# Kernel tuning notes

Measured on AMD Instinct MI355X. Metric: run time of the kernel, lower is better.

## Reference

```python
import jax, jax.numpy as jnp
import numpy as np

N = 200000      # nodes (Elliptic-like AML graph)
E = 400000      # edges
F_IN = 165      # num_features
H = 512         # hidden_units
C = 2           # num_classes


def setup_inputs() -> dict:
    key = jax.random.key(0)
    ks = jax.random.split(key, 10)

    def glorot(k, shape):
        fan_in = shape[0]
        return (jax.random.normal(k, shape, jnp.float32) / np.float32(np.sqrt(fan_in)))

    return {
        "x": jax.random.normal(ks[0], (N, F_IN), jnp.float32),
        "edge_index": jax.random.randint(ks[1], (2, E), 0, N, dtype=jnp.int32),
        # ChebConv1: K=2 -> two weight mats + one bias
        "W1_0": glorot(ks[2], (F_IN, H)),
        "W1_1": glorot(ks[3], (F_IN, H)),
        "b1": jnp.zeros((H,), jnp.float32),
        # ChebConv2: K=2
        "W2_0": glorot(ks[4], (H, H)),
        "W2_1": glorot(ks[5], (H, H)),
        "b2": jnp.zeros((H,), jnp.float32),
        # final Linear
        "Wl": glorot(ks[6], (H, C)),
        "bl": jnp.zeros((C,), jnp.float32),
    }


def _edge_norm(src, dst, n, dtype):
    # Scaled Chebyshev Laplacian L_hat = 2L/lambda_max - I with sym norm and
    # lambda_max=2 (PyG defaults): diagonal is 0, off-diag = -D^{-1/2} A D^{-1/2}.
    ones = jnp.ones(src.shape[0], dtype)
    deg = jax.ops.segment_sum(ones, src, num_segments=n)
    dis = jnp.where(deg > 0, jax.lax.rsqrt(jnp.where(deg > 0, deg, 1.0)), 0.0)
    return -dis[src] * dis[dst]  # [E]


def _prop(h, src, dst, w, n):
    # One application of L_hat: gather -> weight -> scatter-add. [E, F] messages.
    return jax.ops.segment_sum(w[:, None] * h[src], dst, num_segments=n)


def reference(x, edge_index, W1_0, W1_1, b1, W2_0, W2_1, b2, Wl, bl):
    n = x.shape[0]
    src, dst = edge_index[0], edge_index[1]
    w = _edge_norm(src, dst, n, x.dtype)
    # ChebConv K=2: out = Tx0 @ W0 + Tx1 @ W1 + b, Tx1 = L_hat x
    h = jax.nn.relu(x @ W1_0 + _prop(x, src, dst, w, n) @ W1_1 + b1)
    h = jax.nn.relu(h @ W2_0 + _prop(h, src, dst, w, n) @ W2_1 + b2)
    return h @ Wl + bl  # [N, C] logits
```

## Files before the change

### kernel.cpp

```cpp
#include <hip/hip_runtime.h>

#define NNODES 200000
#define MPAD   200064
#define NEDGES 400000
#define FIN    165
#define K1P    192
#define HID    512
#define NB     ((NNODES + 255) / 256)

typedef __bf16 bf16_t;
typedef __bf16 bf16x8 __attribute__((ext_vector_type(8)));
typedef float  f32x4  __attribute__((ext_vector_type(4)));
typedef unsigned short su16x8 __attribute__((ext_vector_type(8)));
typedef float f32x4u __attribute__((ext_vector_type(4), aligned(4)));

static __device__ __forceinline__ float bf2f(unsigned short u) {
    unsigned int x = ((unsigned int)u) << 16;
    return __builtin_bit_cast(float, x);
}
static __device__ __forceinline__ unsigned short f2bf(float f) {
    bf16_t h = (bf16_t)f;
    return __builtin_bit_cast(unsigned short, h);
}
static __device__ __forceinline__ void gl_lds16(const void* g, void* l) {
    __builtin_amdgcn_global_load_lds(
        (const __attribute__((address_space(1))) unsigned int*)g,
        (__attribute__((address_space(3))) unsigned int*)l, 16, 0, 0);
}
static __device__ __forceinline__ int xcd_swz(int i, int nb) {
    int q = nb >> 3, r = nb & 7;
    int xcd = i & 7, seq = i >> 3;
    return (xcd < r ? xcd * (q + 1) : r * (q + 1) + (xcd - r) * q) + seq;
}

__global__ void k_deg(const int* __restrict__ src, const int* __restrict__ dst,
                      int* __restrict__ deg, int* __restrict__ cnt, int E) {
    int e = blockIdx.x * 256 + threadIdx.x;
    if (e < E) {
        atomicAdd(&deg[src[e]], 1);
        atomicAdd(&cnt[dst[e]], 1);
    }
}

__global__ void k_scan1(int* __restrict__ cnt, int* __restrict__ btot, int n) {
    __shared__ int s[256];
    int i = blockIdx.x * 256 + threadIdx.x;
    int v = (i < n) ? cnt[i] : 0;
    s[threadIdx.x] = v;
    __syncthreads();
    #pragma unroll
    for (int off = 1; off < 256; off <<= 1) {
        int t = (threadIdx.x >= off) ? s[threadIdx.x - off] : 0;
        __syncthreads();
        s[threadIdx.x] += t;
        __syncthreads();
    }
    if (i < n) cnt[i] = s[threadIdx.x] - v;
    if (threadIdx.x == 255) btot[blockIdx.x] = s[255];
}

__global__ void k_scan2(int* __restrict__ btot, int nb) {
    __shared__ int s[1024];
    int i = threadIdx.x;
    int v = (i < nb) ? btot[i] : 0;
    s[i] = v;
    __syncthreads();
    #pragma unroll
    for (int off = 1; off < 1024; off <<= 1) {
        int t = (i >= off) ? s[i - off] : 0;
        __syncthreads();
        s[i] += t;
        __syncthreads();
    }
    if (i < nb) btot[i] = s[i] - v;
}

__global__ void k_scan3(int* __restrict__ cnt, const int* __restrict__ btot,
                        int* __restrict__ rowptr, int n, int E) {
    int i = blockIdx.x * 256 + threadIdx.x;
    if (i < n) {
        rowptr[i] = cnt[i] + btot[blockIdx.x];
        cnt[i] = 0;
    }
    if (i == 0) rowptr[n] = E;
}

__global__ void k_scatter(const int* __restrict__ src, const int* __restrict__ dst,
                          const int* __restrict__ rowptr, int* __restrict__ cur,
                          const int* __restrict__ deg, int* __restrict__ esrc,
                          float* __restrict__ ew, float* __restrict__ outinit,
                          const float* __restrict__ bl, int E) {
    int e = blockIdx.x * 256 + threadIdx.x;
    if (e < E) {
        int s = src[e], d = dst[e];
        int pos = rowptr[d] + atomicAdd(&cur[d], 1);
        esrc[pos] = s;
        if (ew) {
            int da = deg[s], db = deg[d];
            float fa = da > 0 ? rsqrtf((float)da) : 0.f;
            float fb = db > 0 ? rsqrtf((float)db) : 0.f;
            ew[pos] = -fa * fb;
        }
        if (outinit) outinit[e] = bl[e & 1];
    }
}

__global__ void k_buildP1(const float* __restrict__ W0, const float* __restrict__ W1,
                          unsigned short* __restrict__ P) {
    int idx = blockIdx.x * 256 + threadIdx.x;
    if (idx >= 2 * K1P * HID) return;
    int panel = idx / (K1P * HID);
    int rem   = idx - panel * (K1P * HID);
    int j  = rem & 7;
    int n  = (rem >> 3) & 511;
    int q  = (rem >> 12) & 3;
    int kt = rem >> 14;
    int k  = kt * 32 + q * 8 + j;
    const float* W = panel ? W1 : W0;
    P[idx] = (k < FIN) ? f2bf(W[(size_t)k * HID + n]) : (unsigned short)0;
}

__global__ void k_buildP(const float* __restrict__ W, unsigned short* __restrict__ P,
                         int kp, int kfull) {
    int idx = blockIdx.x * 256 + threadIdx.x;
    if (idx >= kp * HID) return;
    int j  = idx & 7;
    int n  = (idx >> 3) & 511;
    int q  = (idx >> 12) & 3;
    int kt = idx >> 14;
    int k  = kt * 32 + q * 8 + j;
    P[idx] = (k < kfull) ? f2bf(W[(size_t)k * HID + n]) : (unsigned short)0;
}

__global__ void k_buildP2cat(const float* __restrict__ W0, const float* __restrict__ W1,
                             unsigned short* __restrict__ P) {
    int idx = blockIdx.x * 256 + threadIdx.x;
    if (idx >= 1024 * HID) return;
    int j  = idx & 7;
    int n  = (idx >> 3) & 511;
    int q  = (idx >> 12) & 3;
    int kt = idx >> 14;
    int k  = kt * 32 + q * 8 + j;
    float v = (k < HID) ? W0[(size_t)k * HID + n] : W1[(size_t)(k - HID) * HID + n];
    P[idx] = f2bf(v);
}

__global__ void k_xcvt(const float* __restrict__ x, unsigned short* __restrict__ xb) {
    long i = ((long)blockIdx.x * 256 + threadIdx.x) * 8;
    if (i >= (long)NNODES * K1P) return;
    int row = (int)(i / K1P), k = (int)(i % K1P);
    const float* xr = x + (size_t)row * FIN;
    __align__(16) unsigned short v[8];
    #pragma unroll
    for (int j = 0; j < 8; ++j)
        v[j] = (k + j < FIN) ? f2bf(xr[k + j]) : (unsigned short)0;
    *(su16x8*)&xb[i] = *(su16x8*)v;
}


template<int K, int LDA, int NCMB>
__global__ __launch_bounds__(256, 4)
void k_gemms(const unsigned short* __restrict__ A, const unsigned short* __restrict__ P,
             unsigned short* __restrict__ D0, unsigned short* __restrict__ D1,
             int os0, int os1, int ob0, int ob1) {
    constexpr int KT2 = K / 64;
    __shared__ unsigned short Al[128 * 64];
    __shared__ unsigned short Bl[2][4][1024];

    const int t    = threadIdx.x;
    const int lane = t & 63;
    const int wv   = t >> 6;
    const int wm   = wv >> 1, wn = wv & 1;
    const int wg   = xcd_swz(blockIdx.x, gridDim.x);
    const int combo = wg & (NCMB - 1);
    const int sel  = combo >> 2;
    const int ncol = (combo & 3) * 128;
    const int m0   = (wg / NCMB) * 128;
    const unsigned short* Pb = P + (size_t)sel * K * 512 + ncol * 8;
    unsigned short* D = sel ? D1 : D0;
    const int os = sel ? os1 : os0;
    const int oc = (sel ? ob1 : ob0) + ncol;

    const unsigned short* Ab = A + (size_t)m0 * LDA;
    const int ar0 = t >> 3;
    const int ach = t & 7;

    f32x4 acc[4][4];
    #pragma unroll
    for (int m = 0; m < 4; ++m)
        #pragma unroll
        for (int n = 0; n < 4; ++n)
            acc[m][n] = (f32x4){0.f, 0.f, 0.f, 0.f};

    for (int kt = 0; kt < KT2; ++kt) {
        __syncthreads();
        #pragma unroll
        for (int i = 0; i < 4; ++i) {
            int r = i * 32 + ar0;
            gl_lds16(Ab + (size_t)r * LDA + kt * 64 + (ach ^ (r & 7)) * 8,
                     &Al[i * 2048 + t * 8]);
        }
        #pragma unroll
        for (int h = 0; h < 2; ++h)
            #pragma unroll
            for (int i = 0; i < 2; ++i)
                gl_lds16(Pb + (size_t)(kt * 2 + h) * 16384 + wv * 4096 + lane * 8 + i * 512,
                         &Bl[h][wv][lane * 8 + i * 512]);
        __syncthreads();

        const int kq = lane >> 4;
        #pragma unroll
        for (int ks = 0; ks < 2; ++ks) {
            bf16x8 af[4], bfr[4];
            #pragma unroll
            for (int m = 0; m < 4; ++m) {
                int r = wm * 64 + m * 16 + (lane & 15);
                int c = ks * 4 + kq;
                af[m] = *(const bf16x8*)&Al[r * 64 + (c ^ (r & 7)) * 8];
            }
            #pragma unroll
            for (int n = 0; n < 4; ++n) {
                int c = wn * 64 + n * 16 + (lane & 15);
                bfr[n] = *(const bf16x8*)&Bl[ks][kq][c * 8];
            }
            #pragma unroll
            for (int m = 0; m < 4; ++m)
                #pragma unroll
                for (int n = 0; n < 4; ++n)
                    acc[m][n] = __builtin_amdgcn_mfma_f32_16x16x32_bf16(bfr[n], af[m], acc[m][n], 0, 0, 0);
        }
    }

    #pragma unroll
    for (int m = 0; m < 4; ++m) {
        int r = m0 + wm * 64 + m * 16 + (lane & 15);
        #pragma unroll
        for (int n = 0; n < 4; ++n) {
            int cb = oc + wn * 64 + n * 16 + (lane >> 4) * 4;
            uint2 pk;
            pk.x = ((unsigned int)f2bf(acc[m][n][1]) << 16) | (unsigned int)f2bf(acc[m][n][0]);
            pk.y = ((unsigned int)f2bf(acc[m][n][3]) << 16) | (unsigned int)f2bf(acc[m][n][2]);
            *(uint2*)&D[(size_t)r * os + cb] = pk;
        }
    }
}

__global__ __launch_bounds__(256, 4)
void k_gemmf(const unsigned short* __restrict__ A0, const unsigned short* __restrict__ A1,
             const unsigned short* __restrict__ P, const float* __restrict__ b2,
             const float* __restrict__ Wl, float* __restrict__ out) {
    constexpr int KT2 = 16;
    __shared__ unsigned short Al[128 * 64];
    __shared__ unsigned short Bl[2][4][1024];

    const int t    = threadIdx.x;
    const int lane = t & 63;
    const int wv   = t >> 6;
    const int wm   = wv >> 1, wn = wv & 1;
    const int wg   = xcd_swz(blockIdx.x, gridDim.x);
    const int ncol = (wg & 3) * 128;
    const int m0   = (wg >> 2) * 128;
    const unsigned short* Pb = P + ncol * 8;
    const int ar0 = t >> 3, ach = t & 7;

    f32x4 acc[4][4];
    #pragma unroll
    for (int m = 0; m < 4; ++m)
        #pragma unroll
        for (int n = 0; n < 4; ++n)
            acc[m][n] = (f32x4){0.f, 0.f, 0.f, 0.f};

    for (int kt = 0; kt < KT2; ++kt) {
        const unsigned short* Ab = (kt < 8 ? A0 : A1) + (size_t)m0 * 512 + (kt & 7) * 64;
        __syncthreads();
        #pragma unroll
        for (int i = 0; i < 4; ++i) {
            int r = i * 32 + ar0;
            gl_lds16(Ab + (size_t)r * 512 + (ach ^ (r & 7)) * 8,
                     &Al[i * 2048 + t * 8]);
        }
        #pragma unroll
        for (int h = 0; h < 2; ++h)
            #pragma unroll
            for (int i = 0; i < 2; ++i)
                gl_lds16(Pb + (size_t)(kt * 2 + h) * 16384 + wv * 4096 + lane * 8 + i * 512,
                         &Bl[h][wv][lane * 8 + i * 512]);
        __syncthreads();

        const int kq = lane >> 4;
        #pragma unroll
        for (int ks = 0; ks < 2; ++ks) {
            bf16x8 af[4], bfr[4];
            #pragma unroll
            for (int m = 0; m < 4; ++m) {
                int r = wm * 64 + m * 16 + (lane & 15);
                int c = ks * 4 + kq;
                af[m] = *(const bf16x8*)&Al[r * 64 + (c ^ (r & 7)) * 8];
            }
            #pragma unroll
            for (int n = 0; n < 4; ++n) {
                int c = wn * 64 + n * 16 + (lane & 15);
                bfr[n] = *(const bf16x8*)&Bl[ks][kq][c * 8];
            }
            #pragma unroll
            for (int m = 0; m < 4; ++m)
                #pragma unroll
                for (int n = 0; n < 4; ++n)
                    acc[m][n] = __builtin_amdgcn_mfma_f32_16x16x32_bf16(bfr[n], af[m], acc[m][n], 0, 0, 0);
        }
    }

    float s0[4] = {0.f, 0.f, 0.f, 0.f}, s1[4] = {0.f, 0.f, 0.f, 0.f};
    #pragma unroll
    for (int n = 0; n < 4; ++n) {
        int cg = ncol + wn * 64 + n * 16 + (lane >> 4) * 4;
        float4 bb   = *(const float4*)(b2 + cg);
        float4 wl01 = *(const float4*)(Wl + (size_t)cg * 2);
        float4 wl23 = *(const float4*)(Wl + (size_t)cg * 2 + 4);
        float b2v[4] = {bb.x, bb.y, bb.z, bb.w};
        float w0v[4] = {wl01.x, wl01.z, wl23.x, wl23.z};
        float w1v[4] = {wl01.y, wl01.w, wl23.y, wl23.w};
        #pragma unroll
        for (int m = 0; m < 4; ++m)
            #pragma unroll
            for (int j = 0; j < 4; ++j) {
                float z = acc[m][n][j] + b2v[j];
                z = z > 0.f ? z : 0.f;
                s0[m] += z * w0v[j];
                s1[m] += z * w1v[j];
            }
    }
    #pragma unroll
    for (int m = 0; m < 4; ++m) {
        s0[m] += __shfl_xor(s0[m], 16, 64);
        s0[m] += __shfl_xor(s0[m], 32, 64);
        s1[m] += __shfl_xor(s1[m], 16, 64);
        s1[m] += __shfl_xor(s1[m], 32, 64);
    }
    if (lane < 16) {
        #pragma unroll
        for (int m = 0; m < 4; ++m) {
            int r = m0 + wm * 64 + m * 16 + lane;
            if (r < NNODES) {
                unsafeAtomicAdd(&out[2 * (size_t)r],     s0[m]);
                unsafeAtomicAdd(&out[2 * (size_t)r + 1], s1[m]);
            }
        }
    }
}

__global__ __launch_bounds__(512, 1)
void k_gemmw(const unsigned short* __restrict__ A, const unsigned short* __restrict__ P,
             unsigned short* __restrict__ U, int ooff, int M) {
    constexpr int KT = HID / 32;
    __shared__ unsigned short Al[2][128 * 32];
    __shared__ unsigned short Bl[2][4][HID * 8];

    const int t    = threadIdx.x;
    const int lane = t & 63;
    const int wv   = t >> 6;
    const int wm   = wv >> 2, wn = wv & 3;
    const int m0   = blockIdx.x * 128;

    const int srow = t >> 2;
    const int gch  = ((t & 3) ^ ((srow >> 1) & 3)) * 8;
    const unsigned short* Ab = A + (size_t)(m0 + srow) * 1024 + gch;
    const bool rok = (m0 + srow) < M;
    const unsigned short* Pb = P + (size_t)t * 8;

    f32x4 acc[4][8];
    #pragma unroll
    for (int m = 0; m < 4; ++m)
        #pragma unroll
        for (int n = 0; n < 8; ++n)
            acc[m][n] = (f32x4){0.f, 0.f, 0.f, 0.f};

    if (rok) gl_lds16(Ab, &Al[0][t * 8]);
    #pragma unroll
    for (int q = 0; q < 4; ++q) gl_lds16(Pb + q * 4096, &Bl[0][q][t * 8]);
    __syncthreads();

    int cur = 0;
    for (int kt = 0; kt < KT; ++kt) {
        if (kt + 1 < KT) {
            if (rok) gl_lds16(Ab + (kt + 1) * 32, &Al[cur ^ 1][t * 8]);
            const unsigned short* Pn = Pb + (size_t)(kt + 1) * 16384;
            #pragma unroll
            for (int q = 0; q < 4; ++q)
                gl_lds16(Pn + q * 4096, &Bl[cur ^ 1][q][t * 8]);
        }
        bf16x8 af[4], bfr[8];
        #pragma unroll
        for (int m = 0; m < 4; ++m) {
            int r  = wm * 64 + m * 16 + (lane & 15);
            int kq = lane >> 4;
            af[m] = *(const bf16x8*)&Al[cur][r * 32 + 8 * (kq ^ ((r >> 1) & 3))];
        }
        #pragma unroll
        for (int n = 0; n < 8; ++n) {
            int c = wn * 128 + n * 16 + (lane & 15);
            bfr[n] = *(const bf16x8*)&Bl[cur][lane >> 4][c * 8];
        }
        #pragma unroll
        for (int m = 0; m < 4; ++m)
            #pragma unroll
            for (int n = 0; n < 8; ++n)
                acc[m][n] = __builtin_amdgcn_mfma_f32_16x16x32_bf16(bfr[n], af[m], acc[m][n], 0, 0, 0);
        __syncthreads();
        cur ^= 1;
    }

    #pragma unroll
    for (int m = 0; m < 4; ++m) {
        int r = m0 + wm * 64 + m * 16 + (lane & 15);
        if (r < M) {
            #pragma unroll
            for (int n = 0; n < 8; ++n) {
                int cb = ooff + wn * 128 + n * 16 + (lane >> 4) * 4;
                uint2 pk;
                pk.x = ((unsigned int)f2bf(acc[m][n][1]) << 16) | (unsigned int)f2bf(acc[m][n][0]);
                pk.y = ((unsigned int)f2bf(acc[m][n][3]) << 16) | (unsigned int)f2bf(acc[m][n][2]);
                *(uint2*)&U[(size_t)r * 1024 + cb] = pk;
            }
        }
    }
}

__global__ __launch_bounds__(512, 1)
void k_gemm0(const float* __restrict__ Aptr, const unsigned short* __restrict__ P,
             unsigned short* __restrict__ U, int ooff, int M) {
    constexpr int K  = K1P;
    constexpr int KT = K / 32;
    __shared__ unsigned short Al[128 * 32];
    __shared__ unsigned short Bpl[4][HID * 8];

    const int t    = threadIdx.x;
    const int lane = t & 63;
    const int wv   = t >> 6;
    const int wm   = wv >> 2, wn = wv & 3;
    const int m0   = blockIdx.x * 128;

    f32x4 acc[4][8];
    #pragma unroll
    for (int m = 0; m < 4; ++m)
        #pragma unroll
        for (int n = 0; n < 8; ++n)
            acc[m][n] = (f32x4){0.f, 0.f, 0.f, 0.f};

    const int srow = t >> 2, sch = t & 3;
    const bool rok = (m0 + srow) < M;

    for (int kt = 0; kt < KT; ++kt) {
        const int k0 = kt * 32;
        __syncthreads();
        {
            const int gk = k0 + sch * 8;
            su16x8 av;
            float f[8];
            const float* Ab = Aptr + (size_t)(m0 + srow) * FIN + gk;
            if (rok && gk + 8 <= FIN) {
                f32x4u lo = *(const f32x4u*)Ab;
                f32x4u hi = *(const f32x4u*)(Ab + 4);
                f[0]=lo.x; f[1]=lo.y; f[2]=lo.z; f[3]=lo.w;
                f[4]=hi.x; f[5]=hi.y; f[6]=hi.z; f[7]=hi.w;
            } else {
                #pragma unroll
                for (int j = 0; j < 8; ++j)
                    f[j] = (rok && gk + j < FIN) ? Ab[j] : 0.f;
            }
            #pragma unroll
            for (int j = 0; j < 8; ++j) av[j] = f2bf(f[j]);
            *(su16x8*)&Al[srow * 32 + 8 * (sch ^ ((srow >> 1) & 3))] = av;
        }
        {
            const unsigned short* Pb = P + (size_t)kt * 16384 + t * 8;
            #pragma unroll
            for (int q = 0; q < 4; ++q)
                *(su16x8*)&Bpl[q][t * 8] = *(const su16x8*)(Pb + q * 4096);
        }
        __syncthreads();
        bf16x8 af[4], bfr[8];
        #pragma unroll
        for (int m = 0; m < 4; ++m) {
            int r  = wm * 64 + m * 16 + (lane & 15);
            int kq = lane >> 4;
            af[m] = *(const bf16x8*)&Al[r * 32 + 8 * (kq ^ ((r >> 1) & 3))];
        }
        #pragma unroll
        for (int n = 0; n < 8; ++n) {
            int c = wn * 128 + n * 16 + (lane & 15);
            bfr[n] = *(const bf16x8*)&Bpl[lane >> 4][c * 8];
        }
        #pragma unroll
        for (int m = 0; m < 4; ++m)
            #pragma unroll
            for (int n = 0; n < 8; ++n)
                acc[m][n] = __builtin_amdgcn_mfma_f32_16x16x32_bf16(bfr[n], af[m], acc[m][n], 0, 0, 0);
    }

    #pragma unroll
    for (int m = 0; m < 4; ++m) {
        int r = m0 + wm * 64 + m * 16 + (lane & 15);
        if (r < M) {
            #pragma unroll
            for (int n = 0; n < 8; ++n) {
                int cb = ooff + wn * 128 + n * 16 + (lane >> 4) * 4;
                uint2 pk;
                pk.x = ((unsigned int)f2bf(acc[m][n][1]) << 16) | (unsigned int)f2bf(acc[m][n][0]);
                pk.y = ((unsigned int)f2bf(acc[m][n][3]) << 16) | (unsigned int)f2bf(acc[m][n][2]);
                *(uint2*)&U[(size_t)r * 1024 + cb] = pk;
            }
        }
    }
}

__global__ void k_aggrh1(unsigned short* __restrict__ dbuf, const unsigned short* __restrict__ gbuf,
                         const int* __restrict__ rowptr, const int* __restrict__ esrc,
                         const float* __restrict__ ew, const float* __restrict__ bias, int M) {
    int wid  = (blockIdx.x * 256 + threadIdx.x) >> 6;
    int lane = threadIdx.x & 63;
    if (wid >= M) return;
    int e0 = rowptr[wid], e1 = rowptr[wid + 1];

    unsigned short* u0 = dbuf + (size_t)wid * 512 + lane * 8;
    uint4 v0 = *(const uint4*)u0;
    unsigned int a0[4] = {v0.x, v0.y, v0.z, v0.w};
    float acc[8], ac2[8];
    #pragma unroll
    for (int i = 0; i < 4; ++i) {
        acc[2 * i]     = bf2f((unsigned short)(a0[i] & 0xffffu));
        acc[2 * i + 1] = bf2f((unsigned short)(a0[i] >> 16));
        ac2[2 * i] = 0.f; ac2[2 * i + 1] = 0.f;
    }
    int e = e0;
    for (; e + 1 < e1; e += 2) {
        int sa = esrc[e], sb = esrc[e + 1];
        float wa = ew[e], wb = ew[e + 1];
        const uint4 va = *(const uint4*)(gbuf + (size_t)sa * 512 + lane * 8);
        const uint4 vb = *(const uint4*)(gbuf + (size_t)sb * 512 + lane * 8);
        unsigned int ua[4] = {va.x, va.y, va.z, va.w};
        unsigned int ub[4] = {vb.x, vb.y, vb.z, vb.w};
        #pragma unroll
        for (int i = 0; i < 4; ++i) {
            acc[2 * i]     += wa * bf2f((unsigned short)(ua[i] & 0xffffu));
            acc[2 * i + 1] += wa * bf2f((unsigned short)(ua[i] >> 16));
            ac2[2 * i]     += wb * bf2f((unsigned short)(ub[i] & 0xffffu));
            ac2[2 * i + 1] += wb * bf2f((unsigned short)(ub[i] >> 16));
        }
    }
    if (e < e1) {
        int sa = esrc[e];
        float wa = ew[e];
        const uint4 va = *(const uint4*)(gbuf + (size_t)sa * 512 + lane * 8);
        unsigned int ua[4] = {va.x, va.y, va.z, va.w};
        #pragma unroll
        for (int i = 0; i < 4; ++i) {
            acc[2 * i]     += wa * bf2f((unsigned short)(ua[i] & 0xffffu));
            acc[2 * i + 1] += wa * bf2f((unsigned short)(ua[i] >> 16));
        }
    }
    float4 c0 = *(const float4*)(bias + lane * 8);
    float4 c1 = *(const float4*)(bias + lane * 8 + 4);
    float bb[8] = {c0.x,c0.y,c0.z,c0.w,c1.x,c1.y,c1.z,c1.w};
    #pragma unroll
    for (int i = 0; i < 8; ++i) {
        float f = acc[i] + ac2[i] + bb[i];
        acc[i] = f > 0.f ? f : 0.f;
    }
    uint4 w4;
    unsigned int* wo = (unsigned int*)&w4;
    #pragma unroll
    for (int i = 0; i < 4; ++i)
        wo[i] = ((unsigned int)f2bf(acc[2 * i + 1]) << 16) | (unsigned int)f2bf(acc[2 * i]);
    *(uint4*)u0 = w4;
}

__global__ void k_aggrh2(unsigned short* __restrict__ dbuf, const unsigned short* __restrict__ gbuf,
                         const int* __restrict__ rowptr, const int* __restrict__ esrc,
                         const float* __restrict__ ew, int M) {
    int wid  = (blockIdx.x * 256 + threadIdx.x) >> 6;
    int lane = threadIdx.x & 63;
    if (wid >= M) return;
    int e0 = rowptr[wid], e1 = rowptr[wid + 1];

    float acc[8] = {0.f,0.f,0.f,0.f,0.f,0.f,0.f,0.f};
    float ac2[8] = {0.f,0.f,0.f,0.f,0.f,0.f,0.f,0.f};
    int e = e0;
    for (; e + 1 < e1; e += 2) {
        int sa = esrc[e], sb = esrc[e + 1];
        float wa = ew[e], wb = ew[e + 1];
        const uint4 va = *(const uint4*)(gbuf + (size_t)sa * 512 + lane * 8);
        const uint4 vb = *(const uint4*)(gbuf + (size_t)sb * 512 + lane * 8);
        unsigned int ua[4] = {va.x, va.y, va.z, va.w};
        unsigned int ub[4] = {vb.x, vb.y, vb.z, vb.w};
        #pragma unroll
        for (int i = 0; i < 4; ++i) {
            acc[2 * i]     += wa * bf2f((unsigned short)(ua[i] & 0xffffu));
            acc[2 * i + 1] += wa * bf2f((unsigned short)(ua[i] >> 16));
            ac2[2 * i]     += wb * bf2f((unsigned short)(ub[i] & 0xffffu));
            ac2[2 * i + 1] += wb * bf2f((unsigned short)(ub[i] >> 16));
        }
    }
    if (e < e1) {
        int sa = esrc[e];
        float wa = ew[e];
        const uint4 va = *(const uint4*)(gbuf + (size_t)sa * 512 + lane * 8);
        unsigned int ua[4] = {va.x, va.y, va.z, va.w};
        #pragma unroll
        for (int i = 0; i < 4; ++i) {
            acc[2 * i]     += wa * bf2f((unsigned short)(ua[i] & 0xffffu));
            acc[2 * i + 1] += wa * bf2f((unsigned short)(ua[i] >> 16));
        }
    }
    uint4 w4;
    unsigned int* wo = (unsigned int*)&w4;
    #pragma unroll
    for (int i = 0; i < 4; ++i)
        wo[i] = ((unsigned int)f2bf(acc[2 * i + 1] + ac2[2 * i + 1]) << 16) |
                 (unsigned int)f2bf(acc[2 * i] + ac2[2 * i]);
    *(uint4*)(dbuf + (size_t)wid * 512 + lane * 8) = w4;
}

template<int RELU>
__global__ void k_aggr(unsigned short* U, const int* __restrict__ rowptr,
                       const int* __restrict__ esrc, const int* __restrict__ deg,
                       const float* __restrict__ bias, int M) {
    int wid  = (blockIdx.x * 256 + threadIdx.x) >> 6;
    int lane = threadIdx.x & 63;
    if (wid >= M) return;
    int e0 = rowptr[wid], e1 = rowptr[wid + 1];
    if (RELU == 0 && e0 == e1) return;

    unsigned short* u0 = U + (size_t)wid * 1024 + lane * 8;
    uint4 v0 = *(const uint4*)u0;
    unsigned int a0[4] = {v0.x, v0.y, v0.z, v0.w};
    float acc[8];
    #pragma unroll
    for (int i = 0; i < 4; ++i) {
        acc[2 * i]     = bf2f((unsigned short)(a0[i] & 0xffffu));
        acc[2 * i + 1] = bf2f((unsigned short)(a0[i] >> 16));
    }
    if (e0 < e1) {
        int dd = deg[wid];
        float dr = dd > 0 ? rsqrtf((float)dd) : 0.f;
        for (int e = e0; e < e1; ++e) {
            int s = esrc[e];
            float we = -dr * rsqrtf((float)deg[s]);
            const uint4 v = *(const uint4*)(U + (size_t)s * 1024 + 512 + lane * 8);
            unsigned int uu[4] = {v.x, v.y, v.z, v.w};
            #pragma unroll
            for (int i = 0; i < 4; ++i) {
                acc[2 * i]     += we * bf2f((unsigned short)(uu[i] & 0xffffu));
                acc[2 * i + 1] += we * bf2f((unsigned short)(uu[i] >> 16));
            }
        }
    }
    if (RELU) {
        float4 c0 = *(const float4*)(bias + lane * 8);
        float4 c1 = *(const float4*)(bias + lane * 8 + 4);
        float bb[8] = {c0.x,c0.y,c0.z,c0.w,c1.x,c1.y,c1.z,c1.w};
        #pragma unroll
        for (int i = 0; i < 8; ++i) {
            float f = acc[i] + bb[i];
            acc[i] = f > 0.f ? f : 0.f;
        }
    }
    uint4 w4;
    unsigned int* wo = (unsigned int*)&w4;
    #pragma unroll
    for (int i = 0; i < 4; ++i)
        wo[i] = ((unsigned int)f2bf(acc[2 * i + 1]) << 16) | (unsigned int)f2bf(acc[2 * i]);
    *(uint4*)u0 = w4;
}

__global__ void k_final(const unsigned short* __restrict__ U, const float* __restrict__ b2,
                        const float* __restrict__ Wl, const float* __restrict__ bl,
                        float* __restrict__ out, int M) {
    int wid  = (blockIdx.x * 256 + threadIdx.x) >> 6;
    int lane = threadIdx.x & 63;
    if (wid >= M) return;
    const uint4 v = *(const uint4*)(U + (size_t)wid * 1024 + lane * 8);
    float4 c0 = *(const float4*)(b2 + lane * 8);
    float4 c1 = *(const float4*)(b2 + lane * 8 + 4);
    float bb[8] = {c0.x,c0.y,c0.z,c0.w,c1.x,c1.y,c1.z,c1.w};
    const float4* Wp = reinterpret_cast<const float4*>(Wl + lane * 16);
    float4 w0 = Wp[0], w1 = Wp[1], w2 = Wp[2], w3 = Wp[3];
    float wv[16] = {w0.x, w0.y, w0.z, w0.w, w1.x, w1.y, w1.z, w1.w,
                    w2.x, w2.y, w2.z, w2.w, w3.x, w3.y, w3.z, w3.w};
    unsigned int uu[4] = {v.x, v.y, v.z, v.w};
    float s0 = 0.f, s1 = 0.f;
    #pragma unroll
    for (int j = 0; j < 4; ++j) {
        float f0 = bf2f((unsigned short)(uu[j] & 0xffffu)) + bb[2 * j];
        float f1 = bf2f((unsigned short)(uu[j] >> 16))     + bb[2 * j + 1];
        f0 = f0 > 0.f ? f0 : 0.f;
        f1 = f1 > 0.f ? f1 : 0.f;
        s0 += f0 * wv[4 * j + 0];
        s1 += f0 * wv[4 * j + 1];
        s0 += f1 * wv[4 * j + 2];
        s1 += f1 * wv[4 * j + 3];
    }
    #pragma unroll
    for (int off = 32; off; off >>= 1) {
        s0 += __shfl_xor(s0, off, 64);
        s1 += __shfl_xor(s1, off, 64);
    }
    if (lane == 0) {
        out[2 * (size_t)wid]     = s0 + bl[0];
        out[2 * (size_t)wid + 1] = s1 + bl[1];
    }
}

extern "C" void kernel_launch(void* const* d_in, const int* in_sizes, int n_in,
                              void* d_out, int out_size, void* d_ws, size_t ws_size,
                              hipStream_t stream) {
    const float* x    = (const float*)d_in[0];
    const int*   ei   = (const int*)d_in[1];
    const float* W1_0 = (const float*)d_in[2];
    const float* W1_1 = (const float*)d_in[3];
    const float* b1   = (const float*)d_in[4];
    const float* W2_0 = (const float*)d_in[5];
    const float* W2_1 = (const float*)d_in[6];
    const float* b2   = (const float*)d_in[7];
    const float* Wl   = (const float*)d_in[8];
    const float* bl   = (const float*)d_in[9];
    const int* src = ei;
    const int* dst = ei + NEDGES;
    float* out = (float*)d_out;

    char* ws = (char*)d_ws;
    size_t off = 0;
    auto alloc = [&](size_t bytes) -> void* {
        void* p = ws + off;
        off += (bytes + 255) & ~(size_t)255;
        return p;
    };
    int*            deg    = (int*)alloc((size_t)NNODES * 4);
    int*            cnt    = (int*)alloc((size_t)NNODES * 4);
    int*            rowptr = (int*)alloc((size_t)(NNODES + 1) * 4);
    int*            btot   = (int*)alloc((size_t)NB * 4);
    unsigned short* P1     = (unsigned short*)alloc((size_t)2 * K1P * HID * 2);
    unsigned short* P2     = (unsigned short*)alloc((size_t)2 * HID * HID * 2);
    unsigned short* Hbuf   = (unsigned short*)alloc((size_t)MPAD * 1024 * 2);
    unsigned short* H0 = Hbuf;
    unsigned short* H1 = Hbuf + (size_t)MPAD * 512;
    unsigned short* U  = Hbuf;

    bool esrc_ws = (off + (size_t)NEDGES * 8 <= ws_size);
    int*   esrc = esrc_ws ? (int*)alloc((size_t)NEDGES * 4)   : (int*)d_out;
    float* ew   = esrc_ws ? (float*)alloc((size_t)NEDGES * 4) : nullptr;
    bool have_xb = (off + (size_t)MPAD * K1P * 2 <= ws_size);
    unsigned short* xb = have_xb ? (unsigned short*)alloc((size_t)MPAD * K1P * 2) : nullptr;

    hipMemsetAsync(deg, 0, (size_t)NNODES * 4, stream);
    hipMemsetAsync(cnt, 0, (size_t)NNODES * 4, stream);

    k_deg    <<<(NEDGES + 255) / 256, 256, 0, stream>>>(src, dst, deg, cnt, NEDGES);
    k_scan1  <<<NB, 256, 0, stream>>>(cnt, btot, NNODES);
    k_scan2  <<<1, 1024, 0, stream>>>(btot, NB);
    k_scan3  <<<NB, 256, 0, stream>>>(cnt, btot, rowptr, NNODES, NEDGES);
    k_scatter<<<(NEDGES + 255) / 256, 256, 0, stream>>>(src, dst, rowptr, cnt, deg, esrc,
                                                        ew, esrc_ws ? out : nullptr, bl, NEDGES);

    k_buildP1<<<(2 * K1P * HID + 255) / 256, 256, 0, stream>>>(W1_0, W1_1, P1);
    if (esrc_ws) {
        k_buildP2cat<<<(1024 * HID + 255) / 256, 256, 0, stream>>>(W2_0, W2_1, P2);
    } else {
        const int pg2 = (HID * HID + 255) / 256;
        k_buildP<<<pg2, 256, 0, stream>>>(W2_0, P2, HID, HID);
        k_buildP<<<pg2, 256, 0, stream>>>(W2_1, P2 + (size_t)HID * HID, HID, HID);
    }

    const int nblk = MPAD / 128;

    if (esrc_ws && have_xb) {
        k_xcvt<<<(int)(((long)NNODES * K1P / 8 + 255) / 256), 256, 0, stream>>>(x, xb);
        k_gemms<K1P, K1P, 8><<<8 * nblk, 256, 0, stream>>>(xb, P1, H0, H1, 512, 512, 0, 0);
        k_aggrh1<<<NNODES / 4, 256, 0, stream>>>(H0, H1, rowptr, esrc, ew, b1, NNODES);
        k_aggrh2<<<NNODES / 4, 256, 0, stream>>>(H1, H0, rowptr, esrc, ew, NNODES);
        k_gemmf<<<4 * nblk, 256, 0, stream>>>(H0, H1, P2, b2, Wl, out);
    } else {
        if (have_xb) {
            k_xcvt<<<(int)(((long)NNODES * K1P / 8 + 255) / 256), 256, 0, stream>>>(x, xb);
            k_gemms<K1P, K1P, 8><<<8 * nblk, 256, 0, stream>>>(xb, P1, U, U, 1024, 1024, 0, 512);
        } else {
            k_gemm0<<<nblk, 512, 0, stream>>>(x, P1, U, 0, NNODES);
            k_gemm0<<<nblk, 512, 0, stream>>>(x, P1 + (size_t)K1P * HID, U, 512, NNODES);
        }
        k_aggr<1><<<NNODES / 4, 256, 0, stream>>>(U, rowptr, esrc, deg, b1, NNODES);
        k_gemms<HID, 1024, 4><<<4 * nblk, 256, 0, stream>>>(U, P2 + (size_t)HID * HID,
                                                            U, U, 1024, 1024, 512, 512);
        k_gemmw<<<nblk, 512, 0, stream>>>(U, P2, U, 0, NNODES);
        k_aggr<0><<<NNODES / 4, 256, 0, stream>>>(U, rowptr, esrc, deg, nullptr, NNODES);
        k_final<<<NNODES / 4, 256, 0, stream>>>(U, b2, Wl, bl, out, NNODES);
    }
}
```

Baseline: 774.9 us.

## Double-buffer LDS in final GEMM with vmcnt-based prefetch pipeline

The final fused GEMM kernel now keeps two LDS buffers for the A and B tiles and prefetches the tile two k-steps ahead with direct global-to-LDS loads. Explicit s_waitcnt vmcnt waits and raw barriers replace the two __syncthreads per iteration, so memory loads overlap with MFMA compute. LDS usage doubles, and launch bounds drop to 2 blocks per SM, which lowers occupancy. The hand-placed waits rely on each thread issuing exactly eight loads per stage.

Result: slower. 831.5 us (+7.3%).

```diff
diff --git a/kernel.cpp b/kernel.cpp
--- a/kernel.cpp
+++ b/kernel.cpp
@@ -26,6 +26,14 @@
     __builtin_amdgcn_global_load_lds(
         (const __attribute__((address_space(1))) unsigned int*)g,
         (__attribute__((address_space(3))) unsigned int*)l, 16, 0, 0);
+}
+static __device__ __forceinline__ void wait_vmcnt8() {
+    asm volatile("s_waitcnt vmcnt(8)" ::: "memory");
+    __builtin_amdgcn_sched_barrier(0);
+}
+static __device__ __forceinline__ void wait_vmcnt0() {
+    asm volatile("s_waitcnt vmcnt(0)" ::: "memory");
+    __builtin_amdgcn_sched_barrier(0);
 }
 static __device__ __forceinline__ int xcd_swz(int i, int nb) {
     int q = nb >> 3, r = nb & 7;
@@ -157,7 +165,6 @@
     *(su16x8*)&xb[i] = *(su16x8*)v;
 }
 
-
 template<int K, int LDA, int NCMB>
 __global__ __launch_bounds__(256, 4)
 void k_gemms(const unsigned short* __restrict__ A, const unsigned short* __restrict__ P,
@@ -245,13 +252,13 @@
     }
 }
 
-__global__ __launch_bounds__(256, 4)
+__global__ __launch_bounds__(256, 2)
 void k_gemmf(const unsigned short* __restrict__ A0, const unsigned short* __restrict__ A1,
              const unsigned short* __restrict__ P, const float* __restrict__ b2,
              const float* __restrict__ Wl, float* __restrict__ out) {
     constexpr int KT2 = 16;
-    __shared__ unsigned short Al[128 * 64];
-    __shared__ unsigned short Bl[2][4][1024];
+    __shared__ unsigned short Al[2][128 * 64];
+    __shared__ unsigned short Bl[2][2][4][1024];
 
     const int t    = threadIdx.x;
     const int lane = t & 63;
@@ -270,23 +277,22 @@
         for (int n = 0; n < 4; ++n)
             acc[m][n] = (f32x4){0.f, 0.f, 0.f, 0.f};
 
-    for (int kt = 0; kt < KT2; ++kt) {
+    auto stage = [&](int kt, int b) {
         const unsigned short* Ab = (kt < 8 ? A0 : A1) + (size_t)m0 * 512 + (kt & 7) * 64;
-        __syncthreads();
         #pragma unroll
         for (int i = 0; i < 4; ++i) {
             int r = i * 32 + ar0;
             gl_lds16(Ab + (size_t)r * 512 + (ach ^ (r & 7)) * 8,
-                     &Al[i * 2048 + t * 8]);
+                     &Al[b][i * 2048 + t * 8]);
         }
         #pragma unroll
         for (int h = 0; h < 2; ++h)
             #pragma unroll
             for (int i = 0; i < 2; ++i)
                 gl_lds16(Pb + (size_t)(kt * 2 + h) * 16384 + wv * 4096 + lane * 8 + i * 512,
-                         &Bl[h][wv][lane * 8 + i * 512]);
-        __syncthreads();
-
+                         &Bl[b][h][wv][lane * 8 + i * 512]);
+    };
+    auto compute = [&](int b) {
         const int kq = lane >> 4;
         #pragma unroll
         for (int ks = 0; ks < 2; ++ks) {
@@ -295,18 +301,35 @@
             for (int m = 0; m < 4; ++m) {
                 int r = wm * 64 + m * 16 + (lane & 15);
                 int c = ks * 4 + kq;
-                af[m] = *(const bf16x8*)&Al[r * 64 + (c ^ (r & 7)) * 8];
+                af[m] = *(const bf16x8*)&Al[b][r * 64 + (c ^ (r & 7)) * 8];
             }
             #pragma unroll
             for (int n = 0; n < 4; ++n) {
                 int c = wn * 64 + n * 16 + (lane & 15);
-                bfr[n] = *(const bf16x8*)&Bl[ks][kq][c * 8];
+                bfr[n] = *(const bf16x8*)&Bl[b][ks][kq][c * 8];
             }
             #pragma unroll
             for (int m = 0; m < 4; ++m)
                 #pragma unroll
                 for (int n = 0; n < 4; ++n)
                     acc[m][n] = __builtin_amdgcn_mfma_f32_16x16x32_bf16(bfr[n], af[m], acc[m][n], 0, 0, 0);
+        }
+    };
+
+    stage(0, 0);
+    stage(1, 1);
+    wait_vmcnt8();
+    __builtin_amdgcn_s_barrier();
+
+    for (int kt = 0; kt < KT2; ++kt) {
+        const int cur = kt & 1;
+        compute(cur);
+        __builtin_amdgcn_s_barrier();
+        if (kt + 2 < KT2) stage(kt + 2, cur);
+        if (kt + 1 < KT2) {
+            if (kt + 2 < KT2) wait_vmcnt8();
+            else             wait_vmcnt0();
+            __builtin_amdgcn_s_barrier();
         }
     }
 
```
